# Performance work log

Hardware: AMD Instinct MI355X
Metric: run time of the kernel (lower is better)

Reference implementation:

```python
import jax, jax.numpy as jnp
import numpy as np

NUM_BINS = 15       # calibration_cfg['num_prob_bins']
POOL_W = 3          # calibration_cfg['conf_pool_width']
BIN_WIDTH = 1.0 / NUM_BINS  # get_bins(num_prob_bins, 0.0, 1.0)


def _conv(x, w):
    # x: [N,C,H,W], w: [O,I,kh,kw], SAME padding, stride 1
    return jax.lax.conv_general_dilated(
        x, w, (1, 1), 'SAME', dimension_numbers=('NCHW', 'OIHW', 'NCHW'))


def _neighbor_mean(p):
    # agg_neighbors_preds(discrete=False): mean over POOL_W x POOL_W window,
    # border windows averaged over valid pixels only (count_include_pad=False).
    ones_k = jnp.ones((1, 1, POOL_W, POOL_W), p.dtype)
    s = _conv(p, ones_k)
    cnt = _conv(jnp.ones_like(p), ones_k)
    return s / cnt


def setup_inputs() -> dict:
    key = jax.random.key(0)
    k1, k2, k3, k4, k5 = jax.random.split(key, 5)
    N, C, H, W = 32, 3, 512, 512
    context_images = jax.random.normal(k1, (1, N, C, H, W), jnp.float32)
    context_labels = jax.random.uniform(k2, (1, N, 1, H, W), jnp.float32)
    target_logits = jax.random.normal(k3, (1, 1, H, W), jnp.float32)
    # stand-in base_model params (3x3 conv on image + 3x3 conv on LOO label mean)
    w_img = 0.1 * jax.random.normal(k4, (1, C, 3, 3), jnp.float32)
    w_lab = 0.1 * jax.random.normal(k5, (1, 1, 3, 3), jnp.float32)
    return {"context_images": context_images, "context_labels": context_labels,
            "target_logits": target_logits, "w_img": w_img, "w_lab": w_lab}


def reference(context_images, context_labels, target_logits, w_img, w_lab):
    # context_images: [1,N,C,H,W], context_labels: [1,N,1,H,W], target_logits: [1,1,H,W]
    _, N, C, H, W = context_images.shape
    imgs = context_images[0]   # [N,C,H,W] -- each support image is the held-out target once
    labs = context_labels[0]   # [N,1,H,W]

    # --- leave-one-out support predictions (vectorized over the N-iteration loop) ---
    # stand-in base_model: conv(held-out image) + conv(mean of remaining context labels)
    loo_mean = (jnp.sum(labs, axis=0, keepdims=True) - labs) / (N - 1)  # [N,1,H,W]
    support_logits = _conv(imgs, w_img) + _conv(loo_mean, w_lab)        # [N,1,H,W]
    y_probs = jax.nn.sigmoid(support_logits)
    if POOL_W > 1:
        y_probs = _neighbor_mean(y_probs)
    y_true = (labs > 0.5).astype(jnp.float32)                            # [N,1,H,W]

    # --- histogram bin accumulation (update_prob_pixel_meters + prob_bin_stats) ---
    bin_idx = jnp.clip((y_probs / BIN_WIDTH).astype(jnp.int32), 0, NUM_BINS - 1)
    flat_idx = bin_idx.reshape(-1)
    counts = jax.ops.segment_sum(jnp.ones(flat_idx.shape, jnp.float32), flat_idx,
                                 num_segments=NUM_BINS)
    pos = jax.ops.segment_sum(y_true.reshape(-1), flat_idx, num_segments=NUM_BINS)
    bin_freqs = jnp.where(counts > 0, pos / jnp.maximum(counts, 1.0), 0.0)  # [NUM_BINS]

    # --- bin ownership of target probs + gather (get_bin_per_sample) ---
    uncal_probs = jax.nn.sigmoid(target_logits)                 # [1,1,H,W]
    own = jnp.clip((uncal_probs[:, 0] / BIN_WIDTH).astype(jnp.int32),
                   0, NUM_BINS - 1)[:, None]                    # [1,1,H,W]
    return bin_freqs[own]                                       # [1,1,H,W]
```

## Files before the change

kernel.cpp:

```cpp
#include <hip/hip_runtime.h>
#include <hip/hip_bf16.h>

#define NUM_BINS 15
#define N_CTX 32
#define C_IMG 3
#define HGT 512
#define WID 512
#define HW (HGT * WID)

#define EMITW 60
#define NSTRIP 9
#define SEG 32
#define NSEG (HGT / SEG)
#define UNITS_PER_N (NSTRIP * NSEG)
#define TOTAL_UNITS (N_CTX * UNITS_PER_N)

__global__ __launch_bounds__(256) void k_sumlab(const float4* __restrict__ labs,
                                                float4* __restrict__ sumLab,
                                                unsigned int* __restrict__ hist) {
    int i = blockIdx.x * 256 + threadIdx.x;
    if (blockIdx.x == 0 && threadIdx.x < 2 * NUM_BINS) hist[threadIdx.x] = 0u;
    float4 s = make_float4(0.f, 0.f, 0.f, 0.f);
    #pragma unroll
    for (int n = 0; n < N_CTX; ++n) {
        float4 v = labs[(size_t)n * (HW / 4) + i];
        s.x += v.x; s.y += v.y; s.z += v.z; s.w += v.w;
    }
    sumLab[i] = s;
}

__global__ __launch_bounds__(256) void k_main(const float* __restrict__ imgs,
                                              const float* __restrict__ labs,
                                              const float* __restrict__ sumLab,
                                              const float* __restrict__ w_img,
                                              const float* __restrict__ w_lab,
                                              unsigned int* __restrict__ hist) {
    __shared__ unsigned int sh[2 * NUM_BINS];
    const int tid  = threadIdx.x;
    const int lane = tid & 63;
    const int u    = blockIdx.x * 4 + (tid >> 6);
    const int seg   = u % NSEG;
    const int strip = (u / NSEG) % NSTRIP;
    const int n     = u / UNITS_PER_N;
    const int y0 = seg * SEG;
    const int x  = strip * EMITW + lane - 2;
    const bool xv    = (x >= 0) & (x < WID);
    const bool elane = (lane >= 2) & (lane < 2 + EMITW) & (x < WID);
    const bool col3  = (x != 0) & (x != WID - 1);
    const float inv31 = 1.0f / 31.0f;

    if (tid < 2 * NUM_BINS) sh[tid] = 0u;
    __syncthreads();

    float w[4][3][3];
    #pragma unroll
    for (int c = 0; c < 3; ++c)
        #pragma unroll
        for (int i = 0; i < 3; ++i)
            #pragma unroll
            for (int j = 0; j < 3; ++j)
                w[c][i][j] = w_img[c * 9 + i * 3 + j];
    #pragma unroll
    for (int i = 0; i < 3; ++i)
        #pragma unroll
        for (int j = 0; j < 3; ++j)
            w[3][i][j] = w_lab[i * 3 + j];

    const float* p0 = imgs + (size_t)n * C_IMG * HW + (ptrdiff_t)(y0 - 2) * WID + x;
    const float* p1 = p0 + HW;
    const float* p2 = p0 + 2 * HW;
    const float* pl = labs + (size_t)n * HW + (ptrdiff_t)(y0 - 2) * WID + x;
    const float* ps = sumLab + (ptrdiff_t)(y0 - 2) * WID + x;

    float hA2 = 0.f, hA1 = 0.f, hB1 = 0.f;
    float hs2 = 0.f, hs1 = 0.f;
    float lab1 = 0.f, lab2 = 0.f;
    unsigned int ccnt[NUM_BINS], pcnt[NUM_BINS];
    #pragma unroll
    for (int b = 0; b < NUM_BINS; ++b) { ccnt[b] = 0u; pcnt[b] = 0u; }

    int r = y0 - 2;
    #pragma unroll 4
    for (int it = 0; it < SEG + 4; ++it, ++r) {
        const bool rv = (r >= 0) & (r < HGT);
        const bool lv = rv & xv;
        float v0 = 0.f, v1 = 0.f, v2 = 0.f, lb = 0.f, sl = 0.f;
        if (lv) { v0 = *p0; v1 = *p1; v2 = *p2; lb = *pl; sl = *ps; }
        p0 += WID; p1 += WID; p2 += WID; pl += WID; ps += WID;
        const float v3 = (sl - lb) * inv31;

        const float m0 = __shfl_up(v0, 1), q0 = __shfl_down(v0, 1);
        const float m1 = __shfl_up(v1, 1), q1 = __shfl_down(v1, 1);
        const float m2 = __shfl_up(v2, 1), q2 = __shfl_down(v2, 1);
        const float m3 = __shfl_up(v3, 1), q3 = __shfl_down(v3, 1);

        float hA, hB, hC;
        hA  = w[0][0][0]*m0 + w[0][0][1]*v0 + w[0][0][2]*q0;
        hB  = w[0][1][0]*m0 + w[0][1][1]*v0 + w[0][1][2]*q0;
        hC  = w[0][2][0]*m0 + w[0][2][1]*v0 + w[0][2][2]*q0;
        hA += w[1][0][0]*m1 + w[1][0][1]*v1 + w[1][0][2]*q1;
        hB += w[1][1][0]*m1 + w[1][1][1]*v1 + w[1][1][2]*q1;
        hC += w[1][2][0]*m1 + w[1][2][1]*v1 + w[1][2][2]*q1;
        hA += w[2][0][0]*m2 + w[2][0][1]*v2 + w[2][0][2]*q2;
        hB += w[2][1][0]*m2 + w[2][1][1]*v2 + w[2][1][2]*q2;
        hC += w[2][2][0]*m2 + w[2][2][1]*v2 + w[2][2][2]*q2;
        hA += w[3][0][0]*m3 + w[3][0][1]*v3 + w[3][0][2]*q3;
        hB += w[3][1][0]*m3 + w[3][1][1]*v3 + w[3][1][2]*q3;
        hC += w[3][2][0]*m3 + w[3][2][1]*v3 + w[3][2][2]*q3;

        const float z = hA2 + hB1 + hC;
        hA2 = hA1; hA1 = hA; hB1 = hB;

        const int y = r - 1;
        const bool yv = (y >= 0) & (y < HGT);
        const float pr = 1.0f / (1.0f + __expf(-z));
        const float pc = (yv & xv) ? pr : 0.f;
        const float hs = __shfl_up(pc, 1) + pc + __shfl_down(pc, 1);

        const int yc = r - 2;
        const float psum = hs2 + hs1 + hs;
        hs2 = hs1; hs1 = hs;

        const bool row3 = (yc != 0) & (yc != HGT - 1);
        const float c2b = row3 ? (col3 ? (15.0f / 9.0f) : 2.5f)
                               : (col3 ? 2.5f : 3.75f);
        int b = (int)(psum * c2b);
        b = b < 0 ? 0 : (b > NUM_BINS - 1 ? NUM_BINS - 1 : b);
        const bool pos = lab2 > 0.5f;
        lab2 = lab1; lab1 = lb;

        const bool doemit = elane & (it >= 4);
        const unsigned long long posm = __ballot(doemit & pos);
        #pragma unroll
        for (int bb = 0; bb < NUM_BINS; ++bb) {
            unsigned long long m = __ballot(doemit & (b == bb));
            ccnt[bb] += (unsigned int)__popcll(m);
            pcnt[bb] += (unsigned int)__popcll(m & posm);
        }
    }

    if (lane == 0) {
        #pragma unroll
        for (int b = 0; b < NUM_BINS; ++b) {
            if (ccnt[b]) atomicAdd(&sh[b], ccnt[b]);
            if (pcnt[b]) atomicAdd(&sh[NUM_BINS + b], pcnt[b]);
        }
    }
    __syncthreads();
    if (tid < 2 * NUM_BINS) {
        unsigned int v = sh[tid];
        if (v) atomicAdd(&hist[tid], v);
    }
}

__global__ __launch_bounds__(256) void k_out(const float4* __restrict__ tl,
                                             const unsigned int* __restrict__ hist,
                                             float4* __restrict__ out) {
    __shared__ float s_f[NUM_BINS];
    const float BIN_W = (float)(1.0 / 15.0);
    int tid = threadIdx.x;
    if (tid < NUM_BINS) {
        unsigned int c = hist[tid];
        unsigned int p = hist[NUM_BINS + tid];
        s_f[tid] = (c > 0u) ? (float)p / (float)c : 0.0f;
    }
    __syncthreads();
    int i = blockIdx.x * 256 + tid;
    float4 t = tl[i];
    float4 o;
    {
        float pr = 1.0f / (1.0f + expf(-t.x));
        int b = (int)(pr / BIN_W); b = b < 0 ? 0 : (b > NUM_BINS - 1 ? NUM_BINS - 1 : b);
        o.x = s_f[b];
    }
    {
        float pr = 1.0f / (1.0f + expf(-t.y));
        int b = (int)(pr / BIN_W); b = b < 0 ? 0 : (b > NUM_BINS - 1 ? NUM_BINS - 1 : b);
        o.y = s_f[b];
    }
    {
        float pr = 1.0f / (1.0f + expf(-t.z));
        int b = (int)(pr / BIN_W); b = b < 0 ? 0 : (b > NUM_BINS - 1 ? NUM_BINS - 1 : b);
        o.z = s_f[b];
    }
    {
        float pr = 1.0f / (1.0f + expf(-t.w));
        int b = (int)(pr / BIN_W); b = b < 0 ? 0 : (b > NUM_BINS - 1 ? NUM_BINS - 1 : b);
        o.w = s_f[b];
    }
    out[i] = o;
}

extern "C" void kernel_launch(void* const* d_in, const int* in_sizes, int n_in,
                              void* d_out, int out_size, void* d_ws, size_t ws_size,
                              hipStream_t stream) {
    const float* imgs  = (const float*)d_in[0];
    const float* labs  = (const float*)d_in[1];
    const float* tlog  = (const float*)d_in[2];
    const float* w_img = (const float*)d_in[3];
    const float* w_lab = (const float*)d_in[4];
    float* out = (float*)d_out;

    float* sumLab = (float*)d_ws;
    unsigned int* hist = (unsigned int*)((char*)d_ws + (size_t)HW * sizeof(float));

    k_sumlab<<<HW / 4 / 256, 256, 0, stream>>>((const float4*)labs, (float4*)sumLab, hist);

    k_main<<<TOTAL_UNITS / 4, 256, 0, stream>>>(imgs, labs, sumLab, w_img, w_lab, hist);

    k_out<<<HW / 4 / 256, 256, 0, stream>>>((const float4*)tlog, hist, (float4*)out);
}
```

Before: 221.0 us.

## Process eight columns per lane with float4 loads and packed per-lane histogram counters

Each wavefront now covers a full 512-wide row, with every lane computing 8 adjacent columns loaded as two float4 vectors. This removes the overlapping halo strips and the per-element shuffles. The 15-ballot histogram per row is replaced by per-lane 8-bit packed counters, which are reduced with xor shuffles at the end. The segment height is halved, and launch bounds now allow one block per SM. Register pressure rises sharply, which could reduce occupancy, and the 8-bit counters rely on each lane seeing at most 16*8=128 elements per bin so they do not overflow.

```diff
diff --git a/kernel.cpp b/kernel.cpp
--- a/kernel.cpp
+++ b/kernel.cpp
@@ -8,12 +8,9 @@
 #define WID 512
 #define HW (HGT * WID)
 
-#define EMITW 60
-#define NSTRIP 9
-#define SEG 32
+#define SEG 16
 #define NSEG (HGT / SEG)
-#define UNITS_PER_N (NSTRIP * NSEG)
-#define TOTAL_UNITS (N_CTX * UNITS_PER_N)
+#define UNITS (N_CTX * NSEG)
 
 __global__ __launch_bounds__(256) void k_sumlab(const float4* __restrict__ labs,
                                                 float4* __restrict__ sumLab,
@@ -29,25 +26,23 @@
     sumLab[i] = s;
 }
 
-__global__ __launch_bounds__(256) void k_main(const float* __restrict__ imgs,
-                                              const float* __restrict__ labs,
-                                              const float* __restrict__ sumLab,
-                                              const float* __restrict__ w_img,
-                                              const float* __restrict__ w_lab,
-                                              unsigned int* __restrict__ hist) {
+__global__ __launch_bounds__(256, 1) void k_main(const float* __restrict__ imgs,
+                                                 const float* __restrict__ labs,
+                                                 const float* __restrict__ sumLab,
+                                                 const float* __restrict__ w_img,
+                                                 const float* __restrict__ w_lab,
+                                                 unsigned int* __restrict__ hist) {
     __shared__ unsigned int sh[2 * NUM_BINS];
     const int tid  = threadIdx.x;
     const int lane = tid & 63;
     const int u    = blockIdx.x * 4 + (tid >> 6);
-    const int seg   = u % NSEG;
-    const int strip = (u / NSEG) % NSTRIP;
-    const int n     = u / UNITS_PER_N;
-    const int y0 = seg * SEG;
-    const int x  = strip * EMITW + lane - 2;
-    const bool xv    = (x >= 0) & (x < WID);
-    const bool elane = (lane >= 2) & (lane < 2 + EMITW) & (x < WID);
-    const bool col3  = (x != 0) & (x != WID - 1);
+    const int n    = u >> 5;
+    const int seg  = u & (NSEG - 1);
+    const int y0   = seg * SEG;
+    const int x0   = lane * 8;
     const float inv31 = 1.0f / 31.0f;
+    const bool l0  = (lane == 0);
+    const bool l63 = (lane == 63);
 
     if (tid < 2 * NUM_BINS) sh[tid] = 0u;
     __syncthreads();
@@ -66,84 +61,148 @@
         for (int j = 0; j < 3; ++j)
             w[3][i][j] = w_lab[i * 3 + j];
 
-    const float* p0 = imgs + (size_t)n * C_IMG * HW + (ptrdiff_t)(y0 - 2) * WID + x;
-    const float* p1 = p0 + HW;
-    const float* p2 = p0 + 2 * HW;
-    const float* pl = labs + (size_t)n * HW + (ptrdiff_t)(y0 - 2) * WID + x;
-    const float* ps = sumLab + (ptrdiff_t)(y0 - 2) * WID + x;
-
-    float hA2 = 0.f, hA1 = 0.f, hB1 = 0.f;
-    float hs2 = 0.f, hs1 = 0.f;
-    float lab1 = 0.f, lab2 = 0.f;
-    unsigned int ccnt[NUM_BINS], pcnt[NUM_BINS];
-    #pragma unroll
-    for (int b = 0; b < NUM_BINS; ++b) { ccnt[b] = 0u; pcnt[b] = 0u; }
-
-    int r = y0 - 2;
-    #pragma unroll 4
-    for (int it = 0; it < SEG + 4; ++it, ++r) {
-        const bool rv = (r >= 0) & (r < HGT);
-        const bool lv = rv & xv;
-        float v0 = 0.f, v1 = 0.f, v2 = 0.f, lb = 0.f, sl = 0.f;
-        if (lv) { v0 = *p0; v1 = *p1; v2 = *p2; lb = *pl; sl = *ps; }
-        p0 += WID; p1 += WID; p2 += WID; pl += WID; ps += WID;
-        const float v3 = (sl - lb) * inv31;
-
-        const float m0 = __shfl_up(v0, 1), q0 = __shfl_down(v0, 1);
-        const float m1 = __shfl_up(v1, 1), q1 = __shfl_down(v1, 1);
-        const float m2 = __shfl_up(v2, 1), q2 = __shfl_down(v2, 1);
-        const float m3 = __shfl_up(v3, 1), q3 = __shfl_down(v3, 1);
-
-        float hA, hB, hC;
-        hA  = w[0][0][0]*m0 + w[0][0][1]*v0 + w[0][0][2]*q0;
-        hB  = w[0][1][0]*m0 + w[0][1][1]*v0 + w[0][1][2]*q0;
-        hC  = w[0][2][0]*m0 + w[0][2][1]*v0 + w[0][2][2]*q0;
-        hA += w[1][0][0]*m1 + w[1][0][1]*v1 + w[1][0][2]*q1;
-        hB += w[1][1][0]*m1 + w[1][1][1]*v1 + w[1][1][2]*q1;
-        hC += w[1][2][0]*m1 + w[1][2][1]*v1 + w[1][2][2]*q1;
-        hA += w[2][0][0]*m2 + w[2][0][1]*v2 + w[2][0][2]*q2;
-        hB += w[2][1][0]*m2 + w[2][1][1]*v2 + w[2][1][2]*q2;
-        hC += w[2][2][0]*m2 + w[2][2][1]*v2 + w[2][2][2]*q2;
-        hA += w[3][0][0]*m3 + w[3][0][1]*v3 + w[3][0][2]*q3;
-        hB += w[3][1][0]*m3 + w[3][1][1]*v3 + w[3][1][2]*q3;
-        hC += w[3][2][0]*m3 + w[3][2][1]*v3 + w[3][2][2]*q3;
-
-        const float z = hA2 + hB1 + hC;
-        hA2 = hA1; hA1 = hA; hB1 = hB;
+    const float* pi0 = imgs + (size_t)n * C_IMG * HW + x0;
+    const float* pi1 = pi0 + HW;
+    const float* pi2 = pi0 + 2 * HW;
+    const float* pla = labs + (size_t)n * HW + x0;
+    const float* psu = sumLab + x0;
+
+    float hA2[8], hA1[8], hB1[8], hs2[8], hs1[8], la1[8], la2[8];
+    #pragma unroll
+    for (int c = 0; c < 8; ++c) {
+        hA2[c] = hA1[c] = hB1[c] = 0.f;
+        hs2[c] = hs1[c] = 0.f;
+        la1[c] = la2[c] = 0.f;
+    }
+    unsigned int accC[4] = {0u, 0u, 0u, 0u};
+    unsigned int accP[4] = {0u, 0u, 0u, 0u};
+
+    #pragma unroll 2
+    for (int it = 0; it < SEG + 4; ++it) {
+        const int r = y0 - 2 + it;
+        float4 A0, B0, A1, B1, A2, B2, AL, BL, AS, BS;
+        if (r >= 0 && r < HGT) {
+            const size_t ro = (size_t)r * WID;
+            A0 = *reinterpret_cast<const float4*>(pi0 + ro);
+            B0 = *reinterpret_cast<const float4*>(pi0 + ro + 4);
+            A1 = *reinterpret_cast<const float4*>(pi1 + ro);
+            B1 = *reinterpret_cast<const float4*>(pi1 + ro + 4);
+            A2 = *reinterpret_cast<const float4*>(pi2 + ro);
+            B2 = *reinterpret_cast<const float4*>(pi2 + ro + 4);
+            AL = *reinterpret_cast<const float4*>(pla + ro);
+            BL = *reinterpret_cast<const float4*>(pla + ro + 4);
+            AS = *reinterpret_cast<const float4*>(psu + ro);
+            BS = *reinterpret_cast<const float4*>(psu + ro + 4);
+        } else {
+            const float4 z4 = make_float4(0.f, 0.f, 0.f, 0.f);
+            A0 = B0 = A1 = B1 = A2 = B2 = AL = BL = AS = BS = z4;
+        }
+
+        float v[4][10];
+        v[0][1] = A0.x; v[0][2] = A0.y; v[0][3] = A0.z; v[0][4] = A0.w;
+        v[0][5] = B0.x; v[0][6] = B0.y; v[0][7] = B0.z; v[0][8] = B0.w;
+        v[1][1] = A1.x; v[1][2] = A1.y; v[1][3] = A1.z; v[1][4] = A1.w;
+        v[1][5] = B1.x; v[1][6] = B1.y; v[1][7] = B1.z; v[1][8] = B1.w;
+        v[2][1] = A2.x; v[2][2] = A2.y; v[2][3] = A2.z; v[2][4] = A2.w;
+        v[2][5] = B2.x; v[2][6] = B2.y; v[2][7] = B2.z; v[2][8] = B2.w;
+        v[3][1] = (AS.x - AL.x) * inv31;
+        v[3][2] = (AS.y - AL.y) * inv31;
+        v[3][3] = (AS.z - AL.z) * inv31;
+        v[3][4] = (AS.w - AL.w) * inv31;
+        v[3][5] = (BS.x - BL.x) * inv31;
+        v[3][6] = (BS.y - BL.y) * inv31;
+        v[3][7] = (BS.z - BL.z) * inv31;
+        v[3][8] = (BS.w - BL.w) * inv31;
+        #pragma unroll
+        for (int p = 0; p < 4; ++p) {
+            float lft = __shfl_up(v[p][8], 1);
+            float rgt = __shfl_down(v[p][1], 1);
+            v[p][0] = l0  ? 0.f : lft;
+            v[p][9] = l63 ? 0.f : rgt;
+        }
+
+        float h0[8], h1[8], h2[8];
+        #pragma unroll
+        for (int c = 0; c < 8; ++c) { h0[c] = 0.f; h1[c] = 0.f; h2[c] = 0.f; }
+        #pragma unroll
+        for (int p = 0; p < 4; ++p)
+            #pragma unroll
+            for (int c = 0; c < 8; ++c) {
+                h0[c] += w[p][0][0] * v[p][c] + w[p][0][1] * v[p][c + 1] + w[p][0][2] * v[p][c + 2];
+                h1[c] += w[p][1][0] * v[p][c] + w[p][1][1] * v[p][c + 1] + w[p][1][2] * v[p][c + 2];
+                h2[c] += w[p][2][0] * v[p][c] + w[p][2][1] * v[p][c + 1] + w[p][2][2] * v[p][c + 2];
+            }
 
         const int y = r - 1;
         const bool yv = (y >= 0) & (y < HGT);
-        const float pr = 1.0f / (1.0f + __expf(-z));
-        const float pc = (yv & xv) ? pr : 0.f;
-        const float hs = __shfl_up(pc, 1) + pc + __shfl_down(pc, 1);
-
-        const int yc = r - 2;
-        const float psum = hs2 + hs1 + hs;
-        hs2 = hs1; hs1 = hs;
-
-        const bool row3 = (yc != 0) & (yc != HGT - 1);
-        const float c2b = row3 ? (col3 ? (15.0f / 9.0f) : 2.5f)
-                               : (col3 ? 2.5f : 3.75f);
-        int b = (int)(psum * c2b);
-        b = b < 0 ? 0 : (b > NUM_BINS - 1 ? NUM_BINS - 1 : b);
-        const bool pos = lab2 > 0.5f;
-        lab2 = lab1; lab1 = lb;
-
-        const bool doemit = elane & (it >= 4);
-        const unsigned long long posm = __ballot(doemit & pos);
-        #pragma unroll
-        for (int bb = 0; bb < NUM_BINS; ++bb) {
-            unsigned long long m = __ballot(doemit & (b == bb));
-            ccnt[bb] += (unsigned int)__popcll(m);
-            pcnt[bb] += (unsigned int)__popcll(m & posm);
-        }
-    }
-
-    if (lane == 0) {
-        #pragma unroll
-        for (int b = 0; b < NUM_BINS; ++b) {
-            if (ccnt[b]) atomicAdd(&sh[b], ccnt[b]);
-            if (pcnt[b]) atomicAdd(&sh[NUM_BINS + b], pcnt[b]);
+        float pc_[8];
+        #pragma unroll
+        for (int c = 0; c < 8; ++c) {
+            float z = hA2[c] + hB1[c] + h2[c];
+            float pr = 1.0f / (1.0f + __expf(-z));
+            pc_[c] = yv ? pr : 0.f;
+        }
+        #pragma unroll
+        for (int c = 0; c < 8; ++c) { hA2[c] = hA1[c]; hA1[c] = h0[c]; hB1[c] = h1[c]; }
+
+        float hsv[8];
+        {
+            float lft = __shfl_up(pc_[7], 1);
+            float rgt = __shfl_down(pc_[0], 1);
+            float pl_ = l0  ? 0.f : lft;
+            float pr_ = l63 ? 0.f : rgt;
+            hsv[0] = pl_ + pc_[0] + pc_[1];
+            #pragma unroll
+            for (int c = 1; c < 7; ++c) hsv[c] = pc_[c - 1] + pc_[c] + pc_[c + 1];
+            hsv[7] = pc_[6] + pc_[7] + pr_;
+        }
+
+        if (it >= 4) {
+            const int yc = r - 2;
+            const bool row3 = (yc != 0) & (yc != HGT - 1);
+            const float cbi = row3 ? (15.0f / 9.0f) : 2.5f;
+            const float cbe = row3 ? 2.5f : 3.75f;
+            const float cb0 = l0  ? cbe : cbi;
+            const float cb7 = l63 ? cbe : cbi;
+            #pragma unroll
+            for (int c = 0; c < 8; ++c) {
+                const float psum = hs2[c] + hs1[c] + hsv[c];
+                const float cb = (c == 0) ? cb0 : ((c == 7) ? cb7 : cbi);
+                int b = (int)(psum * cb);
+                b = b > NUM_BINS - 1 ? NUM_BINS - 1 : b;
+                const unsigned int inc = 1u << ((b & 3) << 3);
+                const int rs = b >> 2;
+                const bool pos = la2[c] > 0.5f;
+                const unsigned int incp = pos ? inc : 0u;
+                #pragma unroll
+                for (int k = 0; k < 4; ++k) {
+                    const bool m = (rs == k);
+                    accC[k] += m ? inc : 0u;
+                    accP[k] += m ? incp : 0u;
+                }
+            }
+        }
+
+        #pragma unroll
+        for (int c = 0; c < 8; ++c) { hs2[c] = hs1[c]; hs1[c] = hsv[c]; }
+        la2[0] = la1[0]; la2[1] = la1[1]; la2[2] = la1[2]; la2[3] = la1[3];
+        la2[4] = la1[4]; la2[5] = la1[5]; la2[6] = la1[6]; la2[7] = la1[7];
+        la1[0] = AL.x; la1[1] = AL.y; la1[2] = AL.z; la1[3] = AL.w;
+        la1[4] = BL.x; la1[5] = BL.y; la1[6] = BL.z; la1[7] = BL.w;
+    }
+
+    #pragma unroll
+    for (int b = 0; b < NUM_BINS; ++b) {
+        unsigned int c = (accC[b >> 2] >> ((b & 3) * 8)) & 0xffu;
+        unsigned int p = (accP[b >> 2] >> ((b & 3) * 8)) & 0xffu;
+        #pragma unroll
+        for (int off = 1; off < 64; off <<= 1) {
+            c += __shfl_xor(c, off);
+            p += __shfl_xor(p, off);
+        }
+        if (lane == 0) {
+            atomicAdd(&sh[b], c);
+            atomicAdd(&sh[NUM_BINS + b], p);
         }
     }
     __syncthreads();
@@ -206,7 +265,7 @@
 
     k_sumlab<<<HW / 4 / 256, 256, 0, stream>>>((const float4*)labs, (float4*)sumLab, hist);
 
-    k_main<<<TOTAL_UNITS / 4, 256, 0, stream>>>(imgs, labs, sumLab, w_img, w_lab, hist);
+    k_main<<<UNITS / 4, 256, 0, stream>>>(imgs, labs, sumLab, w_img, w_lab, hist);
 
     k_out<<<HW / 4 / 256, 256, 0, stream>>>((const float4*)tlog, hist, (float4*)out);
 }
```

After: 205.2 us. 1.08x faster.
